# Kernel optimization log

Hardware: AMD Instinct MI355X
Metric: run time of the kernel (lower is better)

Reference implementation:

```python
import jax, jax.numpy as jnp
import numpy as np

N_EMBD = 1024
EXPAND = 2
D_INNER = N_EMBD * EXPAND          # 2048
D_STATE = 64
N_HEADS = D_INNER // D_STATE       # 32
HEAD_DIM = D_INNER // N_HEADS      # 64
N_GROUPS = 1
D_CONV = 4
N_LAYERS = 48
BATCH, SEQ = 1, 512
PROJ_SIZE = 2 * D_INNER + N_HEADS + 2 * N_GROUPS * D_STATE  # 4256
EPS = 1e-6


def setup_inputs() -> dict:
    key = jax.random.key(0)
    ks = jax.random.split(key, 6)
    init_std = 0.02
    proj_std = 0.02 / np.sqrt(2 * N_LAYERS)
    return {
        "x": jax.random.normal(ks[0], (BATCH, SEQ, N_EMBD), jnp.float32),
        "norm_scale": jnp.ones((N_EMBD,), jnp.float32),
        "w_in": jax.random.normal(ks[1], (N_EMBD, PROJ_SIZE), jnp.float32) * init_std,
        "conv_weight": jax.random.normal(ks[2], (D_CONV, D_INNER), jnp.float32) * 0.02,
        "conv_bias": jnp.zeros((D_INNER,), jnp.float32),
        "A_log": jnp.log(0.5 + jnp.arange(N_HEADS, dtype=jnp.float32) * 0.5 / N_HEADS),
        "dt_bias": jax.random.normal(ks[3], (N_HEADS,), jnp.float32) * 0.1,
        "w_out": jax.random.normal(ks[4], (D_INNER, N_EMBD), jnp.float32) * proj_std,
    }


def _mamba_fwd(x, norm_scale, w_in, conv_weight, conv_bias, A_log, dt_bias, w_out):
    b, T, _ = x.shape
    residual = x
    # RMSNorm
    xn = x * jax.lax.rsqrt(jnp.mean(x * x, axis=-1, keepdims=True) + EPS) * norm_scale
    # in_proj and split
    proj = xn @ w_in  # (b, T, proj_size)
    gate = proj[..., :D_INNER]
    ssm_in = proj[..., D_INNER:2 * D_INNER]
    dt_raw = proj[..., 2 * D_INNER:2 * D_INNER + N_HEADS]
    gs = N_GROUPS * D_STATE
    B = proj[..., 2 * D_INNER + N_HEADS:2 * D_INNER + N_HEADS + gs].reshape(b, T, N_GROUPS, D_STATE)
    C = proj[..., 2 * D_INNER + N_HEADS + gs:].reshape(b, T, N_GROUPS, D_STATE)
    # causal depthwise short conv (cross-correlation, matching lax.conv semantics)
    xp = jnp.pad(ssm_in, ((0, 0), (D_CONV - 1, 0), (0, 0)))
    conv = conv_bias + sum(conv_weight[k] * xp[:, k:k + T, :] for k in range(D_CONV))
    h = jax.nn.silu(conv)  # (b, T, d_inner)
    dt = jax.nn.softplus(dt_raw + dt_bias)  # (b, T, H)
    A = -jnp.exp(A_log)  # (H,)
    A_bar = jnp.exp(A[None, None, :] * dt)  # (b, T, H)
    # heads / groups
    hpg = N_HEADS // N_GROUPS
    xh = h.reshape(b, T, N_HEADS, HEAD_DIM)
    Bh = jnp.repeat(B, hpg, axis=2)  # (b, T, H, N)
    Ch = jnp.repeat(C, hpg, axis=2)  # (b, T, H, N)
    # Bu[b,t,h,p,n] = B[b,t,h,n] * dt[b,t,h] * x[b,t,h,p]
    Bu = Bh[:, :, :, None, :] * (dt[..., None, None] * xh[..., None])  # (b,T,H,P,N)

    def _binary_op(left, right):
        a_l, b_l = left
        a_r, b_r = right
        return (a_l * a_r, a_r * b_l + b_r)

    # A_bar broadcast to (b,T,H,1,1) so the pair broadcasts against Bu
    _, states = jax.lax.associative_scan(_binary_op, (A_bar[..., None, None], Bu), axis=1)
    y = jnp.einsum('bthpn,bthn->bthp', states, Ch).reshape(b, T, D_INNER)
    y = y * jax.nn.silu(gate)
    y = y @ w_out
    return residual + y


def reference(x, norm_scale, w_in, conv_weight, conv_bias, A_log, dt_bias, w_out):
    return _mamba_fwd(x, norm_scale, w_in, conv_weight, conv_bias, A_log, dt_bias, w_out)
```

## Files before the change

### kernel.cpp

```cpp
#include <hip/hip_runtime.h>
#include <hip/hip_bf16.h>

typedef unsigned short u16;
typedef float f32x4v __attribute__((ext_vector_type(4)));
typedef short short8 __attribute__((ext_vector_type(8)));

#define TSEQ 512
#define EMB  1024
#define DI   2048
#define NH   32
#define DS   64
#define PROJ 4256
#define PROJP 4352
#define NCH  16
#define LCH  32
#define KSPLIT2 4

__device__ __forceinline__ u16 f2bf(float f) {
    union { __hip_bfloat16 h; u16 u; } cv;
    cv.h = __float2bfloat16(f);
    return cv.u;
}
__device__ __forceinline__ unsigned pack2(float a, float b) {
    return (unsigned)f2bf(a) | ((unsigned)f2bf(b) << 16);
}
__device__ __forceinline__ float silu(float v) { return v / (1.f + expf(-v)); }

__device__ __forceinline__ void transpose_tile(
        const float* __restrict__ src, u16* __restrict__ dst,
        int K, int N, int n0, int k0, int tid, float tile[64][68]) {
    const int lr = tid >> 4;
    const int lc = tid & 15;
    #pragma unroll
    for (int ps = 0; ps < 4; ++ps) {
        int r = ps * 16 + lr;
        float4 v;
        if (n0 + lc * 4 + 3 < N) {
            v = *(const float4*)&src[(size_t)(k0 + r) * N + n0 + lc * 4];
        } else {
            float t0 = 0.f, t1 = 0.f, t2 = 0.f, t3 = 0.f;
            int nb = n0 + lc * 4;
            if (nb + 0 < N) t0 = src[(size_t)(k0 + r) * N + nb + 0];
            if (nb + 1 < N) t1 = src[(size_t)(k0 + r) * N + nb + 1];
            if (nb + 2 < N) t2 = src[(size_t)(k0 + r) * N + nb + 2];
            if (nb + 3 < N) t3 = src[(size_t)(k0 + r) * N + nb + 3];
            v = make_float4(t0, t1, t2, t3);
        }
        *(float4*)&tile[r][lc * 4] = v;
    }
    __syncthreads();
    const int kk2 = (tid & 31) * 2;
    const int nr  = tid >> 5;
    #pragma unroll
    for (int ps = 0; ps < 8; ++ps) {
        int n = ps * 8 + nr;
        unsigned o = (unsigned)f2bf(tile[kk2][n]) | ((unsigned)f2bf(tile[kk2 + 1][n]) << 16);
        *(unsigned*)&dst[(size_t)(n0 + n) * K + k0 + kk2] = o;
    }
}

__global__ __launch_bounds__(256) void k_prep(
        const float* __restrict__ w_in, u16* __restrict__ w_inT,
        const float* __restrict__ w_out, u16* __restrict__ w_outT,
        const float* __restrict__ x, const float* __restrict__ scale,
        u16* __restrict__ xnb) {
    __shared__ float tile[64][68];
    const int b = blockIdx.x;
    const int tid = threadIdx.x;
    if (b < 1088) {
        int bx = b % 68, by = b / 68;
        transpose_tile(w_in, w_inT, 1024, PROJ, bx * 64, by * 64, tid, tile);
    } else if (b < 1600) {
        int b2 = b - 1088;
        int bx = b2 % 16, by = b2 / 16;
        transpose_tile(w_out, w_outT, 2048, 1024, bx * 64, by * 64, tid, tile);
    } else {
        int t = b - 1600;
        const float4* xr = (const float4*)(x + (size_t)t * EMB);
        float4 v = xr[tid];
        float ss = v.x * v.x + v.y * v.y + v.z * v.z + v.w * v.w;
        #pragma unroll
        for (int off = 32; off; off >>= 1) ss += __shfl_xor(ss, off);
        if ((tid & 63) == 0) tile[0][tid >> 6] = ss;
        __syncthreads();
        float tot = tile[0][0] + tile[0][1] + tile[0][2] + tile[0][3];
        float inv = rsqrtf(tot * (1.f / EMB) + 1e-6f);
        float4 s = ((const float4*)scale)[tid];
        uint2 o;
        o.x = pack2(v.x * inv * s.x, v.y * inv * s.y);
        o.y = pack2(v.z * inv * s.z, v.w * inv * s.w);
        ((uint2*)xnb)[(size_t)t * 256 + tid] = o;
    }
}

template<int BM, int BN>
__global__ __launch_bounds__(256) void k_gemm(
        const u16* __restrict__ A, int lda,
        const u16* __restrict__ BT, int ldb,
        float* __restrict__ C, int ldc, int Kper) {
    constexpr int WM = BM / 2, WN = BN / 2, FM = WM / 16, FN = WN / 16;
    constexpr int NA = BM * 8 / 256, NB = BN * 8 / 256;
    __shared__ __align__(16) u16 Al[BM][72];
    __shared__ __align__(16) u16 Bl[BN][72];
    const int tid = threadIdx.x;
    const int wid = tid >> 6, lane = tid & 63;
    const int wr = wid >> 1, wc = wid & 1;
    const int ar = lane & 15, kg = lane >> 4;
    const int row0 = blockIdx.y * BM, col0 = blockIdx.x * BN;
    const int kbase = blockIdx.z * Kper;
    const int Mtot = gridDim.y * BM;
    float* Cz = C + (size_t)blockIdx.z * Mtot * ldc;

    short8 ra[NA], rb[NB];
    auto load_stage = [&](int k0) {
        #pragma unroll
        for (int j = 0; j < NA; ++j) {
            int idx = tid + j * 256;
            ra[j] = *(const short8*)(A + (size_t)(row0 + (idx >> 3)) * lda + k0 + (idx & 7) * 8);
        }
        #pragma unroll
        for (int j = 0; j < NB; ++j) {
            int idx = tid + j * 256;
            rb[j] = *(const short8*)(BT + (size_t)(col0 + (idx >> 3)) * ldb + k0 + (idx & 7) * 8);
        }
    };
    auto write_stage = [&]() {
        #pragma unroll
        for (int j = 0; j < NA; ++j) {
            int idx = tid + j * 256;
            *(short8*)&Al[idx >> 3][(idx & 7) * 8] = ra[j];
        }
        #pragma unroll
        for (int j = 0; j < NB; ++j) {
            int idx = tid + j * 256;
            *(short8*)&Bl[idx >> 3][(idx & 7) * 8] = rb[j];
        }
    };

    f32x4v acc[FM][FN] = {};
    const int NT = Kper / 64;
    load_stage(kbase);
    for (int kt = 0; kt < NT; ++kt) {
        write_stage();
        __syncthreads();
        if (kt + 1 < NT) load_stage(kbase + (kt + 1) * 64);
        #pragma unroll
        for (int kk = 0; kk < 2; ++kk) {
            short8 af[FM], bf[FN];
            #pragma unroll
            for (int m = 0; m < FM; ++m)
                af[m] = *(const short8*)&Al[wr * WM + m * 16 + ar][kk * 32 + kg * 8];
            #pragma unroll
            for (int n = 0; n < FN; ++n)
                bf[n] = *(const short8*)&Bl[wc * WN + n * 16 + ar][kk * 32 + kg * 8];
            #pragma unroll
            for (int m = 0; m < FM; ++m)
                #pragma unroll
                for (int n = 0; n < FN; ++n)
                    acc[m][n] = __builtin_amdgcn_mfma_f32_16x16x32_bf16(
                        af[m], bf[n], acc[m][n], 0, 0, 0);
        }
        __syncthreads();
    }
    #pragma unroll
    for (int m = 0; m < FM; ++m)
        #pragma unroll
        for (int n = 0; n < FN; ++n)
            #pragma unroll
            for (int j = 0; j < 4; ++j) {
                int row = row0 + wr * WM + m * 16 + kg * 4 + j;
                int col = col0 + wc * WN + n * 16 + ar;
                Cz[(size_t)row * ldc + col] = acc[m][n][j];
            }
}

__global__ __launch_bounds__(256) void k_reduce_out(
        const float* __restrict__ part, const float* __restrict__ x,
        float* __restrict__ out) {
    int i = blockIdx.x * 256 + threadIdx.x;
    float4 v = ((const float4*)x)[i];
    #pragma unroll
    for (int z = 0; z < KSPLIT2; ++z) {
        float4 p = ((const float4*)part)[(size_t)z * (TSEQ * EMB / 4) + i];
        v.x += p.x; v.y += p.y; v.z += p.z; v.w += p.w;
    }
    ((float4*)out)[i] = v;
}

__global__ __launch_bounds__(256) void k_scan1g(
        const float* __restrict__ proj, const float* __restrict__ cw,
        const float* __restrict__ cb, const float* __restrict__ A_log,
        const float* __restrict__ dt_bias,
        float* __restrict__ Sloc, float* __restrict__ Pcum,
        float* __restrict__ yloc) {
    const int c = blockIdx.x, h = blockIdx.y;
    const int tid = threadIdx.x;
    const int q = tid & 3, p = tid >> 2, n0 = q * 16;
    __shared__ __align__(16) float Blds[LCH][64];
    __shared__ __align__(16) float Clds[LCH][64];
    __shared__ __align__(16) float xt[LCH + 3][64];
    __shared__ float al[LCH], dl[LCH];
    __shared__ float yl[LCH][64];
    for (int i = tid; i < LCH * 64; i += 256) {
        int t = i >> 6, n = i & 63;
        Blds[t][n] = proj[(size_t)(c * LCH + t) * PROJP + 2 * DI + NH + n];
        Clds[t][n] = proj[(size_t)(c * LCH + t) * PROJP + 2 * DI + NH + DS + n];
    }
    for (int i = tid; i < (LCH + 3) * 64; i += 256) {
        int r = i >> 6, n = i & 63;
        int tt = c * LCH - 3 + r;
        xt[r][n] = (tt >= 0) ? proj[(size_t)tt * PROJP + DI + h * 64 + n] : 0.f;
    }
    if (tid < LCH) {
        float z = proj[(size_t)(c * LCH + tid) * PROJP + 2 * DI + h] + dt_bias[h];
        float dt = (z > 20.f) ? z : log1pf(expf(z));
        dl[tid] = dt;
        al[tid] = expf(-expf(A_log[h]) * dt);
    }
    __syncthreads();
    if (tid < LCH) {
        float pr = 1.f;
        #pragma unroll
        for (int k = 0; k < LCH; ++k) if (k <= tid) pr *= al[k];
        Pcum[((size_t)(c * 32 + h)) * LCH + tid] = pr;
    }
    const int ch = h * 64 + p;
    const float cw0 = cw[0 * DI + ch], cw1 = cw[1 * DI + ch];
    const float cw2 = cw[2 * DI + ch], cw3 = cw[3 * DI + ch];
    const float cbv = cb[ch];
    float x0 = xt[0][p], x1 = xt[1][p], x2 = xt[2][p];
    float s[16] = {};
    for (int t = 0; t < LCH; ++t) {
        float x3 = xt[t + 3][p];
        float cv = cbv + cw0 * x0 + cw1 * x1 + cw2 * x2 + cw3 * x3;
        x0 = x1; x1 = x2; x2 = x3;
        float hv = silu(cv);
        float a = al[t];
        float dtx = dl[t] * hv;
        const float4* brow = (const float4*)&Blds[t][n0];
        const float4* crow = (const float4*)&Clds[t][n0];
        float yp = 0.f;
        #pragma unroll
        for (int i4 = 0; i4 < 4; ++i4) {
            float4 b = brow[i4], cc = crow[i4];
            s[i4*4+0] = a * s[i4*4+0] + dtx * b.x; yp += s[i4*4+0] * cc.x;
            s[i4*4+1] = a * s[i4*4+1] + dtx * b.y; yp += s[i4*4+1] * cc.y;
            s[i4*4+2] = a * s[i4*4+2] + dtx * b.z; yp += s[i4*4+2] * cc.z;
            s[i4*4+3] = a * s[i4*4+3] + dtx * b.w; yp += s[i4*4+3] * cc.w;
        }
        yp += __shfl_xor(yp, 1);
        yp += __shfl_xor(yp, 2);
        if (q == 0) yl[t][p] = yp;
    }
    float* dst = Sloc + ((size_t)(c * 32 + h) * 64 + p) * 64 + n0;
    #pragma unroll
    for (int i4 = 0; i4 < 4; ++i4)
        ((float4*)dst)[i4] = make_float4(s[i4*4], s[i4*4+1], s[i4*4+2], s[i4*4+3]);
    __syncthreads();
    for (int i = tid; i < LCH * 64; i += 256) {
        int t = i >> 6, pp = i & 63;
        yloc[(size_t)(c * LCH + t) * DI + h * 64 + pp] = yl[t][pp];
    }
}

__global__ __launch_bounds__(256) void k_scan2(
        const float* __restrict__ Sloc, const float* __restrict__ Pcum,
        float* __restrict__ Sinit) {
    int gid = blockIdx.x * 256 + threadIdx.x;
    int h = gid >> 12, rem = gid & 4095;
    float s = 0.f;
    #pragma unroll
    for (int cc = 0; cc < NCH; ++cc) {
        size_t o = (size_t)(cc * 32 + h) * 4096 + rem;
        Sinit[o] = s;
        s = Pcum[((size_t)(cc * 32 + h)) * LCH + (LCH - 1)] * s + Sloc[o];
    }
}

__global__ __launch_bounds__(256) void k_corr(
        const float* __restrict__ proj, const float* __restrict__ Sinit,
        const float* __restrict__ Pcum, const float* __restrict__ yloc,
        u16* __restrict__ yg) {
    const int c = blockIdx.x, h = blockIdx.y;
    const int tid = threadIdx.x;
    const int q = tid & 3, p = tid >> 2, n0 = q * 16;
    __shared__ __align__(16) float Clds[LCH][64];
    __shared__ __align__(16) float Sl[64][68];
    __shared__ float Pl[LCH];
    __shared__ float yl[LCH][64];
    for (int i = tid; i < LCH * 64; i += 256) {
        int t = i >> 6, n = i & 63;
        Clds[t][n] = proj[(size_t)(c * LCH + t) * PROJP + 2 * DI + NH + DS + n];
    }
    for (int i = tid; i < 4096; i += 256) {
        Sl[i >> 6][i & 63] = Sinit[(size_t)(c * 32 + h) * 4096 + i];
    }
    if (tid < LCH) Pl[tid] = Pcum[((size_t)(c * 32 + h)) * LCH + tid];
    __syncthreads();
    float st[16];
    #pragma unroll
    for (int i4 = 0; i4 < 4; ++i4) {
        float4 v = *(const float4*)&Sl[p][n0 + i4 * 4];
        st[i4*4+0] = v.x; st[i4*4+1] = v.y; st[i4*4+2] = v.z; st[i4*4+3] = v.w;
    }
    for (int t = 0; t < LCH; ++t) {
        const float4* crow = (const float4*)&Clds[t][n0];
        float acc = 0.f;
        #pragma unroll
        for (int i4 = 0; i4 < 4; ++i4) {
            float4 cc4 = crow[i4];
            acc += st[i4*4+0] * cc4.x + st[i4*4+1] * cc4.y
                 + st[i4*4+2] * cc4.z + st[i4*4+3] * cc4.w;
        }
        acc += __shfl_xor(acc, 1);
        acc += __shfl_xor(acc, 2);
        if (q == 0) yl[t][p] = acc * Pl[t];
    }
    __syncthreads();
    for (int i = tid; i < LCH * 64; i += 256) {
        int t = i >> 6, pp = i & 63;
        float y = yloc[(size_t)(c * LCH + t) * DI + h * 64 + pp] + yl[t][pp];
        float g = proj[(size_t)(c * LCH + t) * PROJP + h * 64 + pp];
        yg[(size_t)(c * LCH + t) * DI + h * 64 + pp] = f2bf(y * silu(g));
    }
}

extern "C" void kernel_launch(void* const* d_in, const int* in_sizes, int n_in,
                              void* d_out, int out_size, void* d_ws, size_t ws_size,
                              hipStream_t stream) {
    (void)in_sizes; (void)n_in; (void)out_size; (void)ws_size;
    const float* x       = (const float*)d_in[0];
    const float* nscale  = (const float*)d_in[1];
    const float* w_in    = (const float*)d_in[2];
    const float* conv_w  = (const float*)d_in[3];
    const float* conv_b  = (const float*)d_in[4];
    const float* A_log   = (const float*)d_in[5];
    const float* dt_bias = (const float*)d_in[6];
    const float* w_out   = (const float*)d_in[7];
    float* out = (float*)d_out;

    char* wsp = (char*)d_ws;
    auto alloc = [&](size_t bytes) {
        char* ptr = wsp;
        wsp += (bytes + 255) & ~(size_t)255;
        return ptr;
    };
    u16*   w_inT  = (u16*)  alloc((size_t)PROJP * 1024 * 2);
    u16*   w_outT = (u16*)  alloc((size_t)1024 * 2048 * 2);
    u16*   xnb    = (u16*)  alloc((size_t)512 * 1024 * 2);
    float* proj   = (float*)alloc((size_t)512 * PROJP * 4);
    float* Pcum   = (float*)alloc((size_t)NCH * 32 * LCH * 4);
    float* Sloc   = (float*)alloc((size_t)NCH * 32 * 4096 * 4);
    float* Sinit  = (float*)alloc((size_t)NCH * 32 * 4096 * 4);
    float* yloc   = (float*)alloc((size_t)512 * 2048 * 4);
    u16*   yg     = (u16*)  alloc((size_t)512 * 2048 * 2);
    float* part2  = (float*)alloc((size_t)KSPLIT2 * 512 * 1024 * 4);

    k_prep<<<2112, 256, 0, stream>>>(w_in, w_inT, w_out, w_outT, x, nscale, xnb);
    k_gemm<32, 128><<<dim3(34, 16, 1), 256, 0, stream>>>(
        xnb, 1024, w_inT, 1024, proj, PROJP, 1024);
    k_scan1g<<<dim3(NCH, 32), 256, 0, stream>>>(
        proj, conv_w, conv_b, A_log, dt_bias, Sloc, Pcum, yloc);
    k_scan2<<<512, 256, 0, stream>>>(Sloc, Pcum, Sinit);
    k_corr<<<dim3(NCH, 32), 256, 0, stream>>>(proj, Sinit, Pcum, yloc, yg);
    k_gemm<32, 128><<<dim3(8, 16, KSPLIT2), 256, 0, stream>>>(
        yg, 2048, w_outT, 2048, part2, 1024, 2048 / KSPLIT2);
    k_reduce_out<<<512, 256, 0, stream>>>(part2, x, out);
}
```

Measured before the change: 155.4 us.

## Widen chunk-scan blocks to 1024 threads and precompute conv/silu into shared memory

```diff
diff --git a/kernel.cpp b/kernel.cpp
--- a/kernel.cpp
+++ b/kernel.cpp
@@ -187,7 +187,7 @@
     ((float4*)out)[i] = v;
 }
 
-__global__ __launch_bounds__(256) void k_scan1g(
+__global__ __launch_bounds__(1024) void k_scan1g(
         const float* __restrict__ proj, const float* __restrict__ cw,
         const float* __restrict__ cb, const float* __restrict__ A_log,
         const float* __restrict__ dt_bias,
@@ -195,21 +195,22 @@
         float* __restrict__ yloc) {
     const int c = blockIdx.x, h = blockIdx.y;
     const int tid = threadIdx.x;
-    const int q = tid & 3, p = tid >> 2, n0 = q * 16;
+    const int q = tid & 15, p = tid >> 4, n0 = q * 4;
     __shared__ __align__(16) float Blds[LCH][64];
     __shared__ __align__(16) float Clds[LCH][64];
+    __shared__ __align__(16) float dtxl[LCH][64];
     __shared__ __align__(16) float xt[LCH + 3][64];
     __shared__ float al[LCH], dl[LCH];
     __shared__ float yl[LCH][64];
-    for (int i = tid; i < LCH * 64; i += 256) {
+    for (int i = tid; i < (LCH + 3) * 64; i += 1024) {
+        int r = i >> 6, n = i & 63;
+        int tt = c * LCH - 3 + r;
+        xt[r][n] = (tt >= 0) ? proj[(size_t)tt * PROJP + DI + h * 64 + n] : 0.f;
+    }
+    for (int i = tid; i < LCH * 64; i += 1024) {
         int t = i >> 6, n = i & 63;
         Blds[t][n] = proj[(size_t)(c * LCH + t) * PROJP + 2 * DI + NH + n];
         Clds[t][n] = proj[(size_t)(c * LCH + t) * PROJP + 2 * DI + NH + DS + n];
-    }
-    for (int i = tid; i < (LCH + 3) * 64; i += 256) {
-        int r = i >> 6, n = i & 63;
-        int tt = c * LCH - 3 + r;
-        xt[r][n] = (tt >= 0) ? proj[(size_t)tt * PROJP + DI + h * 64 + n] : 0.f;
     }
     if (tid < LCH) {
         float z = proj[(size_t)(c * LCH + tid) * PROJP + 2 * DI + h] + dt_bias[h];
@@ -218,46 +219,42 @@
         al[tid] = expf(-expf(A_log[h]) * dt);
     }
     __syncthreads();
+    for (int i = tid; i < LCH * 64; i += 1024) {
+        int t = i >> 6, pp = i & 63;
+        int ch = h * 64 + pp;
+        float cv = cb[ch]
+                 + cw[0 * DI + ch] * xt[t][pp]     + cw[1 * DI + ch] * xt[t + 1][pp]
+                 + cw[2 * DI + ch] * xt[t + 2][pp] + cw[3 * DI + ch] * xt[t + 3][pp];
+        dtxl[t][pp] = dl[t] * silu(cv);
+    }
     if (tid < LCH) {
         float pr = 1.f;
         #pragma unroll
         for (int k = 0; k < LCH; ++k) if (k <= tid) pr *= al[k];
         Pcum[((size_t)(c * 32 + h)) * LCH + tid] = pr;
     }
-    const int ch = h * 64 + p;
-    const float cw0 = cw[0 * DI + ch], cw1 = cw[1 * DI + ch];
-    const float cw2 = cw[2 * DI + ch], cw3 = cw[3 * DI + ch];
-    const float cbv = cb[ch];
-    float x0 = xt[0][p], x1 = xt[1][p], x2 = xt[2][p];
-    float s[16] = {};
+    __syncthreads();
+    float4 s = make_float4(0.f, 0.f, 0.f, 0.f);
+    #pragma unroll 4
     for (int t = 0; t < LCH; ++t) {
-        float x3 = xt[t + 3][p];
-        float cv = cbv + cw0 * x0 + cw1 * x1 + cw2 * x2 + cw3 * x3;
-        x0 = x1; x1 = x2; x2 = x3;
-        float hv = silu(cv);
         float a = al[t];
-        float dtx = dl[t] * hv;
-        const float4* brow = (const float4*)&Blds[t][n0];
-        const float4* crow = (const float4*)&Clds[t][n0];
-        float yp = 0.f;
-        #pragma unroll
-        for (int i4 = 0; i4 < 4; ++i4) {
-            float4 b = brow[i4], cc = crow[i4];
-            s[i4*4+0] = a * s[i4*4+0] + dtx * b.x; yp += s[i4*4+0] * cc.x;
-            s[i4*4+1] = a * s[i4*4+1] + dtx * b.y; yp += s[i4*4+1] * cc.y;
-            s[i4*4+2] = a * s[i4*4+2] + dtx * b.z; yp += s[i4*4+2] * cc.z;
-            s[i4*4+3] = a * s[i4*4+3] + dtx * b.w; yp += s[i4*4+3] * cc.w;
-        }
+        float dtx = dtxl[t][p];
+        float4 b = *(const float4*)&Blds[t][n0];
+        float4 cc = *(const float4*)&Clds[t][n0];
+        s.x = a * s.x + dtx * b.x;
+        s.y = a * s.y + dtx * b.y;
+        s.z = a * s.z + dtx * b.z;
+        s.w = a * s.w + dtx * b.w;
+        float yp = s.x * cc.x + s.y * cc.y + s.z * cc.z + s.w * cc.w;
         yp += __shfl_xor(yp, 1);
         yp += __shfl_xor(yp, 2);
+        yp += __shfl_xor(yp, 4);
+        yp += __shfl_xor(yp, 8);
         if (q == 0) yl[t][p] = yp;
     }
-    float* dst = Sloc + ((size_t)(c * 32 + h) * 64 + p) * 64 + n0;
-    #pragma unroll
-    for (int i4 = 0; i4 < 4; ++i4)
-        ((float4*)dst)[i4] = make_float4(s[i4*4], s[i4*4+1], s[i4*4+2], s[i4*4+3]);
-    __syncthreads();
-    for (int i = tid; i < LCH * 64; i += 256) {
+    *(float4*)&Sloc[((size_t)(c * 32 + h) * 64 + p) * 64 + n0] = s;
+    __syncthreads();
+    for (int i = tid; i < LCH * 64; i += 1024) {
         int t = i >> 6, pp = i & 63;
         yloc[(size_t)(c * LCH + t) * DI + h * 64 + pp] = yl[t][pp];
     }
@@ -359,7 +356,7 @@
     k_prep<<<2112, 256, 0, stream>>>(w_in, w_inT, w_out, w_outT, x, nscale, xnb);
     k_gemm<32, 128><<<dim3(34, 16, 1), 256, 0, stream>>>(
         xnb, 1024, w_inT, 1024, proj, PROJP, 1024);
-    k_scan1g<<<dim3(NCH, 32), 256, 0, stream>>>(
+    k_scan1g<<<dim3(NCH, 32), 1024, 0, stream>>>(
         proj, conv_w, conv_b, A_log, dt_bias, Sloc, Pcum, yloc);
     k_scan2<<<512, 256, 0, stream>>>(Sloc, Pcum, Sinit);
     k_corr<<<dim3(NCH, 32), 256, 0, stream>>>(proj, Sinit, Pcum, yloc, yg);
```

Result: slower. 159.7 us (+2.8%).
